# Optimization experiments

Hardware: AMD Instinct MI355X
Metric: run time of the kernel (lower is better)

The kernel has to match this reference:

```python
import jax, jax.numpy as jnp
import numpy as np

TOK, B, DIM, TXT, NT, KS, H = 576, 64, 1024, 512, 1000, 3, 24
SCALE = TXT ** -0.5  # qk_scale = head_dim**-0.5 with head_dim = out_dim = 512


def _layernorm(x, g, b, eps=1e-5):
    m = jnp.mean(x, axis=-1, keepdims=True)
    v = jnp.var(x, axis=-1, keepdims=True)
    return (x - m) * jax.lax.rsqrt(v + eps) * g + b


def _cross_attn(q_in, kv, Wq):
    # q_in: [B,tok,DIM] -> q: [B,tok,TXT]; kv: [B,NT,TXT] serves as both K and V
    q = jnp.einsum('btd,de->bte', q_in, Wq)
    attn = jax.nn.softmax(jnp.einsum('bte,bne->btn', q, kv) * SCALE, axis=-1)
    return jnp.einsum('btn,bne->bte', attn, kv)


def _dwconv(z, w):
    # z: [B,1,H,H], w: [1,1,KS,KS], padding KS//2, stride 1
    return jax.lax.conv_general_dilated(
        z, w, window_strides=(1, 1), padding=((KS // 2, KS // 2), (KS // 2, KS // 2)),
        dimension_numbers=('NCHW', 'OIHW', 'NCHW'))


def setup_inputs() -> dict:
    key = jax.random.key(0)
    ks = jax.random.split(key, 6)
    return {
        'x': jax.random.normal(ks[0], (TOK + 1, B, DIM), jnp.float32),
        'text_fea': jax.random.normal(ks[1], (NT, B, TXT), jnp.float32),
        'ln_q1_g': jnp.ones((DIM,), jnp.float32), 'ln_q1_b': jnp.zeros((DIM,), jnp.float32),
        'ln_q2_g': jnp.ones((DIM,), jnp.float32), 'ln_q2_b': jnp.zeros((DIM,), jnp.float32),
        'ln_kv_g': jnp.ones((TXT,), jnp.float32), 'ln_kv_b': jnp.zeros((TXT,), jnp.float32),
        'Wq1': jax.random.normal(ks[2], (DIM, TXT), jnp.float32) * 0.02,
        'Wq2': jax.random.normal(ks[3], (DIM, TXT), jnp.float32) * 0.02,
        'conv_dw': jax.random.normal(ks[4], (1, 1, KS, KS), jnp.float32) * 0.1,
        'conv_final': jax.random.normal(ks[5], (DIM, TXT), jnp.float32) * 0.02,  # [out,in]
    }


def reference(x, text_fea, ln_q1_g, ln_q1_b, ln_q2_g, ln_q2_b, ln_kv_g, ln_kv_b,
              Wq1, Wq2, conv_dw, conv_final):
    x_cls, xp = x[:1], x[1:]                      # [1,B,DIM], [TOK,B,DIM]
    x_loc = jnp.transpose(xp, (1, 0, 2))          # [B,TOK,DIM]
    kv = _layernorm(jnp.transpose(text_fea, (1, 0, 2)), ln_kv_g, ln_kv_b)  # [B,NT,TXT]

    o1 = _cross_attn(_layernorm(x_loc, ln_q1_g, ln_q1_b), kv, Wq1)  # [B,TOK,TXT]
    o2 = _cross_attn(_layernorm(x_loc, ln_q2_g, ln_q2_b), kv, Wq2)

    x1 = jnp.transpose(o1, (0, 2, 1)).reshape(B, TXT, H, H)
    x2 = jnp.transpose(o2, (0, 2, 1)).reshape(B, TXT, H, H)

    avg_x = jnp.mean(x1, axis=1, keepdims=True)   # [B,1,H,H]
    max_x = jnp.max(x2, axis=1, keepdims=True)
    gate1 = jax.nn.sigmoid(_dwconv(avg_x, conv_dw))
    gate2 = jax.nn.sigmoid(_dwconv(max_x, conv_dw))

    x_se = x1 * gate1 + x2 * gate2                # [B,TXT,H,H]
    y = jnp.einsum('bchw,oc->bohw', x_se, conv_final)  # 1x1 conv, padding 0

    y = jnp.transpose(y.reshape(B, DIM, TOK), (2, 0, 1))  # [TOK,B,DIM]
    return jnp.concatenate([x_cls, y], axis=0)
```

## Files before the change

kernel.cpp:

```cpp
#include <hip/hip_runtime.h>

#define B_    64
#define TOK_  576
#define DIM_  1024
#define TXT_  512
#define NT_   1000
#define NTQ_  1024
#define NTP_  1024
#define H_    24
#define BT_   (B_ * TOK_)
static constexpr float SCALE_ = 0.0441941738241592f;

typedef __bf16 bf16x8 __attribute__((ext_vector_type(8)));
typedef float  f32x4  __attribute__((ext_vector_type(4)));

__device__ __forceinline__ unsigned short f2bf(float f) {
    unsigned u = __float_as_uint(f);
    u += 0x7fffu + ((u >> 16) & 1u);
    return (unsigned short)(u >> 16);
}
__device__ __forceinline__ float bf2f(unsigned short h) {
    return __uint_as_float(((unsigned)h) << 16);
}
__device__ __forceinline__ f32x4 mfma16(bf16x8 a, bf16x8 b, f32x4 c) {
    return __builtin_amdgcn_mfma_f32_16x16x32_bf16(a, b, c, 0, 0, 0);
}
__device__ __forceinline__ void unpack8(uint4 v, float* f) {
    unsigned a0 = v.x, a1 = v.y, a2 = v.z, a3 = v.w;
    f[0] = bf2f((unsigned short)(a0 & 0xffff)); f[1] = bf2f((unsigned short)(a0 >> 16));
    f[2] = bf2f((unsigned short)(a1 & 0xffff)); f[3] = bf2f((unsigned short)(a1 >> 16));
    f[4] = bf2f((unsigned short)(a2 & 0xffff)); f[5] = bf2f((unsigned short)(a2 >> 16));
    f[6] = bf2f((unsigned short)(a3 & 0xffff)); f[7] = bf2f((unsigned short)(a3 >> 16));
}
__device__ __forceinline__ unsigned encmax(float f) {
    unsigned u = __float_as_uint(f);
    return (u & 0x80000000u) ? ~u : (u | 0x80000000u);
}
__device__ __forceinline__ float decmax(unsigned k) {
    unsigned u = (k & 0x80000000u) ? (k ^ 0x80000000u) : ~k;
    return __uint_as_float(u);
}

typedef const __attribute__((address_space(1))) unsigned int* as1_u32p;
typedef __attribute__((address_space(3))) unsigned int* as3_u32p;
__device__ __forceinline__ void gll16(const void* g, void* l) {
    __builtin_amdgcn_global_load_lds((as1_u32p)g, (as3_u32p)l, 16, 0, 0);
}

__global__ void k_prep_wq(const float* __restrict__ wq1, const float* __restrict__ wq2,
                          const float* __restrict__ g1, const float* __restrict__ g2,
                          unsigned short* __restrict__ wqt) {
    __shared__ float tile[64][68];
    int bx = blockIdx.x, t = threadIdx.x;
    int br = bx >> 7, kt = (bx >> 3) & 15, nt = bx & 7;
    const float* wq = br ? wq2 : wq1;
    const float* gg = br ? g2 : g1;
#pragma unroll
    for (int i = 0; i < 4; ++i) {
        int idx4 = t + i * 256;
        int kl = idx4 >> 4, n4 = (idx4 & 15) * 4;
        float gv = gg[kt * 64 + kl];
        float4 v = *reinterpret_cast<const float4*>(wq + (size_t)(kt * 64 + kl) * 512 + nt * 64 + n4);
        tile[kl][n4 + 0] = v.x * gv; tile[kl][n4 + 1] = v.y * gv;
        tile[kl][n4 + 2] = v.z * gv; tile[kl][n4 + 3] = v.w * gv;
    }
    __syncthreads();
#pragma unroll
    for (int i = 0; i < 4; ++i) {
        int idx4 = t + i * 256;
        int nl = idx4 >> 4, k4 = (idx4 & 15) * 4;
        ushort4 o = make_ushort4(f2bf(tile[k4 + 0][nl]), f2bf(tile[k4 + 1][nl]),
                                 f2bf(tile[k4 + 2][nl]), f2bf(tile[k4 + 3][nl]));
        *reinterpret_cast<ushort4*>(wqt + (size_t)br * 512 * 1024 + (size_t)(nt * 64 + nl) * 1024 + kt * 64 + k4) = o;
    }
}

__global__ void k_qbias(const float* __restrict__ wq1, const float* __restrict__ wq2,
                        const float* __restrict__ b1, const float* __restrict__ b2,
                        float* __restrict__ qbias) {
    int br = blockIdx.x >> 3, e0 = (blockIdx.x & 7) * 64;
    int t = threadIdx.x;
    int e = e0 + (t & 63), part = t >> 6;
    const float* wq = br ? wq2 : wq1;
    const float* bb = br ? b2 : b1;
    float s = 0.f;
    for (int d = part * 256; d < part * 256 + 256; ++d) s += bb[d] * wq[(size_t)d * 512 + e];
    __shared__ float red[256];
    red[t] = s;
    __syncthreads();
    if (t < 64) qbias[br * 512 + e0 + t] = red[t] + red[64 + t] + red[128 + t] + red[192 + t];
}

__global__ void k_f2bf(const float* __restrict__ src, unsigned short* __restrict__ dst, int n4) {
    int i = blockIdx.x * blockDim.x + threadIdx.x;
    if (i < n4) {
        float4 v = *reinterpret_cast<const float4*>(src + (size_t)i * 4);
        ushort4 o = make_ushort4(f2bf(v.x), f2bf(v.y), f2bf(v.z), f2bf(v.w));
        *reinterpret_cast<ushort4*>(dst + (size_t)i * 4) = o;
    }
}

__global__ void k_kvln(const float* __restrict__ tf, const float* __restrict__ g,
                       const float* __restrict__ bta, unsigned short* __restrict__ kvn) {
    int row = blockIdx.x;
    int b = row >> 10, n = row & 1023;
    int t = threadIdx.x;
    unsigned short* dst = kvn + ((size_t)b * NTQ_ + n) * TXT_;
    if (n >= NT_) {
        *reinterpret_cast<ushort4*>(dst + t * 4) = make_ushort4(0, 0, 0, 0);
        return;
    }
    const float* src = tf + ((size_t)n * B_ + b) * TXT_;
    float4 v = *reinterpret_cast<const float4*>(src + t * 4);
    float s = v.x + v.y + v.z + v.w;
    float ss = v.x * v.x + v.y * v.y + v.z * v.z + v.w * v.w;
#pragma unroll
    for (int d = 1; d < 64; d <<= 1) { s += __shfl_xor(s, d); ss += __shfl_xor(ss, d); }
    __shared__ float red[4];
    if ((t & 63) == 0) { red[(t >> 6) * 2] = s; red[(t >> 6) * 2 + 1] = ss; }
    __syncthreads();
    s = red[0] + red[2]; ss = red[1] + red[3];
    float m = s * (1.f / TXT_);
    float rs = rsqrtf(ss * (1.f / TXT_) - m * m + 1e-5f);
    int d0 = t * 4;
    ushort4 o = make_ushort4(f2bf((v.x - m) * rs * g[d0 + 0] + bta[d0 + 0]),
                             f2bf((v.y - m) * rs * g[d0 + 1] + bta[d0 + 1]),
                             f2bf((v.z - m) * rs * g[d0 + 2] + bta[d0 + 2]),
                             f2bf((v.w - m) * rs * g[d0 + 3] + bta[d0 + 3]));
    *reinterpret_cast<ushort4*>(dst + d0) = o;
}

__global__ void k_kvt(const unsigned short* __restrict__ kvn, unsigned short* __restrict__ kvt) {
    __shared__ unsigned short tile[64][68];
    int bx = blockIdx.x;
    int b = bx >> 7, rem = bx & 127, et = rem >> 4, nt = rem & 15;
    int t = threadIdx.x;
#pragma unroll
    for (int i = 0; i < 4; ++i) {
        int idx4 = t + i * 256;
        int nl = idx4 >> 4, e4 = (idx4 & 15) * 4;
        int ng = nt * 64 + nl;
        ushort4 v = make_ushort4(0, 0, 0, 0);
        if (ng < NT_) v = *reinterpret_cast<const ushort4*>(kvn + ((size_t)b * NTQ_ + ng) * TXT_ + et * 64 + e4);
        tile[nl][e4 + 0] = v.x; tile[nl][e4 + 1] = v.y; tile[nl][e4 + 2] = v.z; tile[nl][e4 + 3] = v.w;
    }
    __syncthreads();
#pragma unroll
    for (int i = 0; i < 4; ++i) {
        int idx4 = t + i * 256;
        int el = idx4 >> 4, n4 = (idx4 & 15) * 4;
        ushort4 o = make_ushort4(tile[n4 + 0][el], tile[n4 + 1][el], tile[n4 + 2][el], tile[n4 + 3][el]);
        *reinterpret_cast<ushort4*>(kvt + ((size_t)b * TXT_ + et * 64 + el) * NTP_ + nt * 64 + n4) = o;
    }
}

__global__ void k_xln(const float* __restrict__ x, unsigned short* __restrict__ xn) {
    int bt = blockIdx.x;
    int b = bt / TOK_, tk = bt - b * TOK_;
    const float* src = x + ((size_t)(tk + 1) * B_ + b) * DIM_;
    int t = threadIdx.x;
    float4 v = *reinterpret_cast<const float4*>(src + t * 4);
    float s = v.x + v.y + v.z + v.w;
    float ss = v.x * v.x + v.y * v.y + v.z * v.z + v.w * v.w;
#pragma unroll
    for (int d = 1; d < 64; d <<= 1) { s += __shfl_xor(s, d); ss += __shfl_xor(ss, d); }
    __shared__ float red[8];
    if ((t & 63) == 0) { red[t >> 6] = s; red[4 + (t >> 6)] = ss; }
    __syncthreads();
    s = red[0] + red[1] + red[2] + red[3];
    ss = red[4] + red[5] + red[6] + red[7];
    float m = s * (1.f / DIM_);
    float rs = rsqrtf(ss * (1.f / DIM_) - m * m + 1e-5f);
    int d0 = t * 4;
    ushort4 o = make_ushort4(f2bf((v.x - m) * rs), f2bf((v.y - m) * rs),
                             f2bf((v.z - m) * rs), f2bf((v.w - m) * rs));
    *reinterpret_cast<ushort4*>(xn + (size_t)bt * DIM_ + d0) = o;
}

__device__ __forceinline__ void gemm_loop_gll(const unsigned short* __restrict__ A,
                                              const unsigned short* __restrict__ Bp,
                                              int K, unsigned short* a_lds, unsigned short* b_lds,
                                              int tid, f32x4 acc[4][4]) {
    const int l = tid & 63, w = tid >> 6;
    const int l16 = l & 15, lg = l >> 4;
    const int wm = w & 1, wn = w >> 1;
    const f32x4 fz = {0.f, 0.f, 0.f, 0.f};
#pragma unroll
    for (int mt = 0; mt < 4; ++mt)
#pragma unroll
        for (int nt = 0; nt < 4; ++nt) acc[mt][nt] = fz;
    const int lrow = l >> 3;
    const int k8g = (l & 7) ^ lrow;
    const int nk = K >> 6;
    for (int kt = 0; kt < nk; ++kt) {
#pragma unroll
        for (int i = 0; i < 4; ++i) {
            int row = i * 32 + w * 8 + lrow;
            gll16(A + (size_t)row * K + kt * 64 + k8g * 8, &a_lds[(i * 256 + w * 64) * 8]);
        }
#pragma unroll
        for (int i = 0; i < 4; ++i) {
            int row = i * 32 + w * 8 + lrow;
            gll16(Bp + (size_t)row * K + kt * 64 + k8g * 8, &b_lds[(i * 256 + w * 64) * 8]);
        }
        __syncthreads();
#pragma unroll
        for (int kk = 0; kk < 2; ++kk) {
            bf16x8 af[4], bff[4];
#pragma unroll
            for (int mt = 0; mt < 4; ++mt) {
                int row = wm * 64 + mt * 16 + l16;
                int gs = (kk * 4 + lg) ^ (row & 7);
                af[mt] = *reinterpret_cast<const bf16x8*>(a_lds + row * 64 + gs * 8);
            }
#pragma unroll
            for (int nt = 0; nt < 4; ++nt) {
                int row = wn * 64 + nt * 16 + l16;
                int gs = (kk * 4 + lg) ^ (row & 7);
                bff[nt] = *reinterpret_cast<const bf16x8*>(b_lds + row * 64 + gs * 8);
            }
#pragma unroll
            for (int mt = 0; mt < 4; ++mt)
#pragma unroll
                for (int nt = 0; nt < 4; ++nt)
                    acc[mt][nt] = mfma16(af[mt], bff[nt], acc[mt][nt]);
        }
        __syncthreads();
    }
}

__device__ __forceinline__ void gemm_loop96(const unsigned short* __restrict__ A,
                                            const unsigned short* __restrict__ Bp,
                                            int K, unsigned short* a_lds, unsigned short* b_lds,
                                            int tid, f32x4 acc[3][4]) {
    const int l = tid & 63, w = tid >> 6;
    const int l16 = l & 15, lg = l >> 4;
    const int wm = w & 1, wn = w >> 1;
    const f32x4 fz = {0.f, 0.f, 0.f, 0.f};
#pragma unroll
    for (int mt = 0; mt < 3; ++mt)
#pragma unroll
        for (int nt = 0; nt < 4; ++nt) acc[mt][nt] = fz;
    const int lrow = l >> 3;
    const int k8g = (l & 7) ^ lrow;
    const int nk = K >> 6;
    for (int kt = 0; kt < nk; ++kt) {
#pragma unroll
        for (int i = 0; i < 3; ++i) {
            int row = i * 32 + w * 8 + lrow;
            gll16(A + (size_t)row * K + kt * 64 + k8g * 8, &a_lds[(i * 256 + w * 64) * 8]);
        }
#pragma unroll
        for (int i = 0; i < 4; ++i) {
            int row = i * 32 + w * 8 + lrow;
            gll16(Bp + (size_t)row * K + kt * 64 + k8g * 8, &b_lds[(i * 256 + w * 64) * 8]);
        }
        __syncthreads();
#pragma unroll
        for (int kk = 0; kk < 2; ++kk) {
            bf16x8 af[3], bff[4];
#pragma unroll
            for (int mt = 0; mt < 3; ++mt) {
                int row = wm * 48 + mt * 16 + l16;
                int gs = (kk * 4 + lg) ^ (row & 7);
                af[mt] = *reinterpret_cast<const bf16x8*>(a_lds + row * 64 + gs * 8);
            }
#pragma unroll
            for (int nt = 0; nt < 4; ++nt) {
                int row = wn * 64 + nt * 16 + l16;
                int gs = (kk * 4 + lg) ^ (row & 7);
                bff[nt] = *reinterpret_cast<const bf16x8*>(b_lds + row * 64 + gs * 8);
            }
#pragma unroll
            for (int mt = 0; mt < 3; ++mt)
#pragma unroll
                for (int nt = 0; nt < 4; ++nt)
                    acc[mt][nt] = mfma16(af[mt], bff[nt], acc[mt][nt]);
        }
        __syncthreads();
    }
}

__global__ __launch_bounds__(256, 4) void k_qgemm(const unsigned short* __restrict__ xn,
                                                  const unsigned short* __restrict__ wqt,
                                                  const float* __restrict__ qbias,
                                                  unsigned short* __restrict__ qb) {
    int bid = blockIdx.x;
    int vb = (bid & 7) * 288 + (bid >> 3);
    int bn = vb & 3;
    int t = vb >> 2;
    int br = (t >= 288) ? 1 : 0;
    int bm = t - br * 288;
    const unsigned short* A = xn + (size_t)bm * 128 * DIM_;
    const unsigned short* Bp = wqt + (size_t)br * 512 * 1024 + (size_t)bn * 128 * 1024;
    unsigned short* C = qb + (size_t)br * BT_ * TXT_;
    const float* bias = qbias + br * 512;
    __shared__ unsigned short a_lds[128 * 64];
    __shared__ unsigned short b_lds[128 * 64];
    f32x4 acc[4][4];
    gemm_loop_gll(A, Bp, DIM_, a_lds, b_lds, threadIdx.x, acc);
    const int l = threadIdx.x & 63, w = threadIdx.x >> 6;
    const int l16 = l & 15, lg = l >> 4, wm = w & 1, wn = w >> 1;
#pragma unroll
    for (int mt = 0; mt < 4; ++mt)
#pragma unroll
        for (int nt = 0; nt < 4; ++nt) {
            int col = bn * 128 + wn * 64 + nt * 16 + l16;
            float bv = bias[col];
#pragma unroll
            for (int r = 0; r < 4; ++r) {
                int row = bm * 128 + wm * 64 + mt * 16 + lg * 4 + r;
                C[(size_t)row * TXT_ + col] = f2bf((acc[mt][nt][r] + bv) * SCALE_);
            }
        }
}

__global__ __launch_bounds__(256, 4) void k_score(const unsigned short* __restrict__ qbuf,
                                                  const unsigned short* __restrict__ kvn,
                                                  unsigned short* __restrict__ P,
                                                  float* __restrict__ denom, int br) {
    int bid = blockIdx.x;
    int vb = (bid & 7) * 384 + (bid >> 3);
    int tile = vb % 48, b = vb / 48;
    int mt = tile >> 3, nt = tile & 7;
    const unsigned short* A = qbuf + ((size_t)br * BT_ + (size_t)b * TOK_ + mt * 96) * TXT_;
    const unsigned short* Bp = kvn + (size_t)b * NTQ_ * TXT_ + (size_t)nt * 128 * TXT_;
    __shared__ unsigned short a_lds[96 * 64];
    __shared__ unsigned short b_lds[128 * 64];
    f32x4 acc[3][4];
    gemm_loop96(A, Bp, TXT_, a_lds, b_lds, threadIdx.x, acc);
    const int l = threadIdx.x & 63, w = threadIdx.x >> 6;
    const int l16 = l & 15, lg = l >> 4, wm = w & 1, wn = w >> 1;
    float* dn = denom + (size_t)br * BT_;
#pragma unroll
    for (int mt2 = 0; mt2 < 3; ++mt2)
#pragma unroll
        for (int r = 0; r < 4; ++r) {
            int row = b * TOK_ + mt * 96 + wm * 48 + mt2 * 16 + lg * 4 + r;
            float s = 0.f;
#pragma unroll
            for (int nt2 = 0; nt2 < 4; ++nt2) {
                int col = nt * 128 + wn * 64 + nt2 * 16 + l16;
                float p = (col < NT_) ? __expf(acc[mt2][nt2][r]) : 0.f;
                s += p;
                P[(size_t)row * NTP_ + col] = f2bf(p);
            }
#pragma unroll
            for (int d = 1; d < 16; d <<= 1) s += __shfl_xor(s, d);
            if (l16 == 0) atomicAdd(&dn[row], s);
        }
}

__global__ __launch_bounds__(256, 4) void k_pv(const unsigned short* __restrict__ P,
                                               const unsigned short* __restrict__ kvt,
                                               const float* __restrict__ denom,
                                               unsigned short* __restrict__ ob,
                                               float* __restrict__ avgs,
                                               unsigned* __restrict__ maxe, int br) {
    int bid = blockIdx.x;
    int vb = (bid & 7) * 192 + (bid >> 3);
    int tile = vb % 24, b = vb / 24;
    int mt = tile >> 2, nt = tile & 3;
    const unsigned short* A = P + ((size_t)b * TOK_ + mt * 96) * NTP_;
    const unsigned short* Bp = kvt + (size_t)b * TXT_ * NTP_ + (size_t)nt * 128 * NTP_;
    __shared__ unsigned short a_lds[96 * 64];
    __shared__ unsigned short b_lds[128 * 64];
    f32x4 acc[3][4];
    gemm_loop96(A, Bp, NTP_, a_lds, b_lds, threadIdx.x, acc);
    const int l = threadIdx.x & 63, w = threadIdx.x >> 6;
    const int l16 = l & 15, lg = l >> 4, wm = w & 1, wn = w >> 1;
    const float* dn = denom + (size_t)br * BT_;
#pragma unroll
    for (int mt2 = 0; mt2 < 3; ++mt2)
#pragma unroll
        for (int r = 0; r < 4; ++r) {
            int row = b * TOK_ + mt * 96 + wm * 48 + mt2 * 16 + lg * 4 + r;
            float inv = 1.f / dn[row];
            unsigned short* dst = ob + ((size_t)br * BT_ + row) * TXT_;
            float sum = 0.f, mx = -1e30f;
#pragma unroll
            for (int nt2 = 0; nt2 < 4; ++nt2) {
                int col = nt * 128 + wn * 64 + nt2 * 16 + l16;
                float o = acc[mt2][nt2][r] * inv;
                dst[col] = f2bf(o);
                sum += o;
                mx = fmaxf(mx, o);
            }
#pragma unroll
            for (int d = 1; d < 16; d <<= 1) {
                sum += __shfl_xor(sum, d);
                mx = fmaxf(mx, __shfl_xor(mx, d));
            }
            if (l16 == 0) {
                if (br == 0) atomicAdd(&avgs[row], sum);
                else         atomicMax(&maxe[row], encmax(mx));
            }
        }
}

__global__ __launch_bounds__(256, 4) void k_fgemm(const unsigned short* __restrict__ xse,
                                                  const unsigned short* __restrict__ wfb,
                                                  float* __restrict__ out) {
    int bid = blockIdx.x;
    int vb = (bid & 7) * 288 + (bid >> 3);
    int bn = vb & 7, bm = vb >> 3;
    const unsigned short* A = xse + (size_t)bm * 128 * TXT_;
    const unsigned short* Bp = wfb + (size_t)bn * 128 * TXT_;
    __shared__ unsigned short a_lds[128 * 64];
    __shared__ unsigned short b_lds[128 * 64];
    f32x4 acc[4][4];
    gemm_loop_gll(A, Bp, TXT_, a_lds, b_lds, threadIdx.x, acc);
    const int l = threadIdx.x & 63, w = threadIdx.x >> 6;
    const int l16 = l & 15, lg = l >> 4, wm = w & 1, wn = w >> 1;
#pragma unroll
    for (int mt = 0; mt < 4; ++mt)
#pragma unroll
        for (int r = 0; r < 4; ++r) {
            int rowg = bm * 128 + wm * 64 + mt * 16 + lg * 4 + r;
            int b = rowg / TOK_, tk = rowg - b * TOK_;
            float* dst = out + ((size_t)(tk + 1) * B_ + b) * DIM_;
#pragma unroll
            for (int nt = 0; nt < 4; ++nt) {
                int col = bn * 128 + wn * 64 + nt * 16 + l16;
                dst[col] = acc[mt][nt][r];
            }
        }
}

__global__ void k_xse(const unsigned short* __restrict__ o1, const unsigned short* __restrict__ o2,
                      const float* __restrict__ avgs, const unsigned* __restrict__ maxe,
                      const float* __restrict__ cdw, unsigned short* __restrict__ xse) {
    int idx8 = blockIdx.x * 256 + threadIdx.x;
    int bt = idx8 >> 6, e8 = threadIdx.x & 63;
    float gg1 = 0.f, gg2 = 0.f;
    if (e8 == 0) {
        int b = bt / TOK_, hw = bt - b * TOK_, h = hw / H_, ww = hw - h * H_;
        float a1 = 0.f, a2 = 0.f;
#pragma unroll
        for (int ky = 0; ky < 3; ++ky)
#pragma unroll
            for (int kx = 0; kx < 3; ++kx) {
                int hh = h + ky - 1, wx = ww + kx - 1;
                if (hh >= 0 && hh < H_ && wx >= 0 && wx < H_) {
                    float wv = cdw[ky * 3 + kx];
                    int s = b * TOK_ + hh * H_ + wx;
                    a1 += wv * avgs[s] * (1.f / TXT_);
                    a2 += wv * decmax(maxe[s]);
                }
            }
        gg1 = 1.f / (1.f + __expf(-a1));
        gg2 = 1.f / (1.f + __expf(-a2));
    }
    gg1 = __shfl(gg1, 0);
    gg2 = __shfl(gg2, 0);
    float f1[8], f2[8];
    unpack8(*reinterpret_cast<const uint4*>(o1 + (size_t)bt * TXT_ + e8 * 8), f1);
    unpack8(*reinterpret_cast<const uint4*>(o2 + (size_t)bt * TXT_ + e8 * 8), f2);
    unsigned r[4];
#pragma unroll
    for (int j = 0; j < 4; ++j) {
        unsigned lo = f2bf(f1[2 * j] * gg1 + f2[2 * j] * gg2);
        unsigned hi = f2bf(f1[2 * j + 1] * gg1 + f2[2 * j + 1] * gg2);
        r[j] = lo | (hi << 16);
    }
    uint4 o = make_uint4(r[0], r[1], r[2], r[3]);
    *reinterpret_cast<uint4*>(xse + (size_t)bt * TXT_ + e8 * 8) = o;
}

extern "C" void kernel_launch(void* const* d_in, const int* in_sizes, int n_in,
                              void* d_out, int out_size, void* d_ws, size_t ws_size,
                              hipStream_t stream) {
    (void)in_sizes; (void)n_in; (void)out_size; (void)ws_size;
    const float* x    = (const float*)d_in[0];
    const float* tf   = (const float*)d_in[1];
    const float* lq1g = (const float*)d_in[2];
    const float* lq1b = (const float*)d_in[3];
    const float* lq2g = (const float*)d_in[4];
    const float* lq2b = (const float*)d_in[5];
    const float* lkvg = (const float*)d_in[6];
    const float* lkvb = (const float*)d_in[7];
    const float* wq1  = (const float*)d_in[8];
    const float* wq2  = (const float*)d_in[9];
    const float* cdw  = (const float*)d_in[10];
    const float* wf   = (const float*)d_in[11];
    float* out = (float*)d_out;

    char* ws = (char*)d_ws;
    size_t off = 0;
    auto carve = [&](size_t bytes) { char* p = ws + off; off += (bytes + 255) & ~(size_t)255; return p; };
    unsigned short* kvn  = (unsigned short*)carve((size_t)B_ * NTQ_ * TXT_ * 2);
    unsigned short* kvt  = (unsigned short*)carve((size_t)B_ * TXT_ * NTP_ * 2);
    unsigned short* wqt  = (unsigned short*)carve((size_t)2 * 512 * 1024 * 2);
    unsigned short* wfb  = (unsigned short*)carve((size_t)1024 * 512 * 2);
    float* qbias = (float*)carve((size_t)2 * 512 * 4);
    float* denom = (float*)carve((size_t)2 * BT_ * 4);
    float* avgs  = (float*)carve((size_t)BT_ * 4);
    unsigned* maxe = (unsigned*)carve((size_t)BT_ * 4);
    unsigned short* xn   = (unsigned short*)carve((size_t)BT_ * DIM_ * 2);
    unsigned short* qbuf = (unsigned short*)carve((size_t)2 * BT_ * TXT_ * 2);
    unsigned short* ob   = (unsigned short*)carve((size_t)2 * BT_ * TXT_ * 2);
    unsigned short* Pm   = xn;
    unsigned short* xse  = qbuf;

    hipMemcpyAsync(out, x, (size_t)B_ * DIM_ * sizeof(float), hipMemcpyDeviceToDevice, stream);

    k_prep_wq<<<256, 256, 0, stream>>>(wq1, wq2, lq1g, lq2g, wqt);
    k_qbias<<<16, 256, 0, stream>>>(wq1, wq2, lq1b, lq2b, qbias);
    k_f2bf<<<512, 256, 0, stream>>>(wf, wfb, 131072);
    k_kvln<<<B_ * NTQ_, 128, 0, stream>>>(tf, lkvg, lkvb, kvn);
    k_kvt<<<8192, 256, 0, stream>>>(kvn, kvt);
    k_xln<<<BT_, 256, 0, stream>>>(x, xn);
    k_qgemm<<<2304, 256, 0, stream>>>(xn, wqt, qbias, qbuf);
    hipMemsetAsync(denom, 0, (size_t)2 * BT_ * 4, stream);
    hipMemsetAsync(avgs, 0, (size_t)BT_ * 4, stream);
    hipMemsetAsync(maxe, 0, (size_t)BT_ * 4, stream);
    k_score<<<3072, 256, 0, stream>>>(qbuf, kvn, Pm, denom, 0);
    k_pv<<<1536, 256, 0, stream>>>(Pm, kvt, denom, ob, avgs, maxe, 0);
    k_score<<<3072, 256, 0, stream>>>(qbuf, kvn, Pm, denom, 1);
    k_pv<<<1536, 256, 0, stream>>>(Pm, kvt, denom, ob, avgs, maxe, 1);
    k_xse<<<9216, 256, 0, stream>>>(ob, ob + (size_t)BT_ * TXT_, avgs, maxe, cdw, xse);
    k_fgemm<<<2304, 256, 0, stream>>>(xse, wfb, out);
}
```

Before: 636.9 us.

## Fuse gating into final GEMM A-load and use wave-per-row layernorms

Removes the separate xse kernel. The final 1x1-conv GEMM now computes the sigmoid gates per row, loads o1/o2 directly, blends them and writes the bf16 result into LDS as its A tile. This avoids writing and re-reading the xse intermediate. The two layernorm kernels now process one row per wavefront, with 8 rows per block and no LDS reduction or barrier. The three memsets are merged into one. The cost is that A loads become synchronous register loads instead of direct global-to-LDS loads, and the gates are recomputed once per column block (8 times per row).

Result: no change. 635.3 us (-0.3%).

```diff
diff --git a/kernel.cpp b/kernel.cpp
--- a/kernel.cpp
+++ b/kernel.cpp
@@ -100,34 +100,35 @@
     }
 }
 
-__global__ void k_kvln(const float* __restrict__ tf, const float* __restrict__ g,
-                       const float* __restrict__ bta, unsigned short* __restrict__ kvn) {
-    int row = blockIdx.x;
+__global__ __launch_bounds__(512, 2) void k_kvln(const float* __restrict__ tf, const float* __restrict__ g,
+                                                 const float* __restrict__ bta, unsigned short* __restrict__ kvn) {
+    int row = blockIdx.x * 8 + (threadIdx.x >> 6);
     int b = row >> 10, n = row & 1023;
-    int t = threadIdx.x;
-    unsigned short* dst = kvn + ((size_t)b * NTQ_ + n) * TXT_;
+    int l = threadIdx.x & 63;
+    unsigned short* dst = kvn + ((size_t)b * NTQ_ + n) * TXT_ + l * 8;
     if (n >= NT_) {
-        *reinterpret_cast<ushort4*>(dst + t * 4) = make_ushort4(0, 0, 0, 0);
+        *reinterpret_cast<uint4*>(dst) = make_uint4(0, 0, 0, 0);
         return;
     }
-    const float* src = tf + ((size_t)n * B_ + b) * TXT_;
-    float4 v = *reinterpret_cast<const float4*>(src + t * 4);
-    float s = v.x + v.y + v.z + v.w;
-    float ss = v.x * v.x + v.y * v.y + v.z * v.z + v.w * v.w;
+    const float* src = tf + ((size_t)n * B_ + b) * TXT_ + l * 8;
+    float4 v0 = *reinterpret_cast<const float4*>(src);
+    float4 v1 = *reinterpret_cast<const float4*>(src + 4);
+    float s  = v0.x + v0.y + v0.z + v0.w + v1.x + v1.y + v1.z + v1.w;
+    float ss = v0.x * v0.x + v0.y * v0.y + v0.z * v0.z + v0.w * v0.w
+             + v1.x * v1.x + v1.y * v1.y + v1.z * v1.z + v1.w * v1.w;
 #pragma unroll
     for (int d = 1; d < 64; d <<= 1) { s += __shfl_xor(s, d); ss += __shfl_xor(ss, d); }
-    __shared__ float red[4];
-    if ((t & 63) == 0) { red[(t >> 6) * 2] = s; red[(t >> 6) * 2 + 1] = ss; }
-    __syncthreads();
-    s = red[0] + red[2]; ss = red[1] + red[3];
     float m = s * (1.f / TXT_);
     float rs = rsqrtf(ss * (1.f / TXT_) - m * m + 1e-5f);
-    int d0 = t * 4;
-    ushort4 o = make_ushort4(f2bf((v.x - m) * rs * g[d0 + 0] + bta[d0 + 0]),
-                             f2bf((v.y - m) * rs * g[d0 + 1] + bta[d0 + 1]),
-                             f2bf((v.z - m) * rs * g[d0 + 2] + bta[d0 + 2]),
-                             f2bf((v.w - m) * rs * g[d0 + 3] + bta[d0 + 3]));
-    *reinterpret_cast<ushort4*>(dst + d0) = o;
+    float4 g0 = *reinterpret_cast<const float4*>(g + l * 8);
+    float4 g1 = *reinterpret_cast<const float4*>(g + l * 8 + 4);
+    float4 b0 = *reinterpret_cast<const float4*>(bta + l * 8);
+    float4 b1 = *reinterpret_cast<const float4*>(bta + l * 8 + 4);
+    unsigned r0 = (unsigned)f2bf((v0.x - m) * rs * g0.x + b0.x) | ((unsigned)f2bf((v0.y - m) * rs * g0.y + b0.y) << 16);
+    unsigned r1 = (unsigned)f2bf((v0.z - m) * rs * g0.z + b0.z) | ((unsigned)f2bf((v0.w - m) * rs * g0.w + b0.w) << 16);
+    unsigned r2 = (unsigned)f2bf((v1.x - m) * rs * g1.x + b1.x) | ((unsigned)f2bf((v1.y - m) * rs * g1.y + b1.y) << 16);
+    unsigned r3 = (unsigned)f2bf((v1.z - m) * rs * g1.z + b1.z) | ((unsigned)f2bf((v1.w - m) * rs * g1.w + b1.w) << 16);
+    *reinterpret_cast<uint4*>(dst) = make_uint4(r0, r1, r2, r3);
 }
 
 __global__ void k_kvt(const unsigned short* __restrict__ kvn, unsigned short* __restrict__ kvt) {
@@ -154,27 +155,33 @@
     }
 }
 
-__global__ void k_xln(const float* __restrict__ x, unsigned short* __restrict__ xn) {
-    int bt = blockIdx.x;
+__global__ __launch_bounds__(512, 2) void k_xln(const float* __restrict__ x, unsigned short* __restrict__ xn) {
+    int bt = blockIdx.x * 8 + (threadIdx.x >> 6);
     int b = bt / TOK_, tk = bt - b * TOK_;
-    const float* src = x + ((size_t)(tk + 1) * B_ + b) * DIM_;
-    int t = threadIdx.x;
-    float4 v = *reinterpret_cast<const float4*>(src + t * 4);
-    float s = v.x + v.y + v.z + v.w;
-    float ss = v.x * v.x + v.y * v.y + v.z * v.z + v.w * v.w;
+    int l = threadIdx.x & 63;
+    const float* src = x + ((size_t)(tk + 1) * B_ + b) * DIM_ + l * 16;
+    float4 v[4];
+#pragma unroll
+    for (int j = 0; j < 4; ++j) v[j] = *reinterpret_cast<const float4*>(src + j * 4);
+    float s = 0.f, ss = 0.f;
+#pragma unroll
+    for (int j = 0; j < 4; ++j) {
+        s += v[j].x + v[j].y + v[j].z + v[j].w;
+        ss += v[j].x * v[j].x + v[j].y * v[j].y + v[j].z * v[j].z + v[j].w * v[j].w;
+    }
 #pragma unroll
     for (int d = 1; d < 64; d <<= 1) { s += __shfl_xor(s, d); ss += __shfl_xor(ss, d); }
-    __shared__ float red[8];
-    if ((t & 63) == 0) { red[t >> 6] = s; red[4 + (t >> 6)] = ss; }
-    __syncthreads();
-    s = red[0] + red[1] + red[2] + red[3];
-    ss = red[4] + red[5] + red[6] + red[7];
     float m = s * (1.f / DIM_);
     float rs = rsqrtf(ss * (1.f / DIM_) - m * m + 1e-5f);
-    int d0 = t * 4;
-    ushort4 o = make_ushort4(f2bf((v.x - m) * rs), f2bf((v.y - m) * rs),
-                             f2bf((v.z - m) * rs), f2bf((v.w - m) * rs));
-    *reinterpret_cast<ushort4*>(xn + (size_t)bt * DIM_ + d0) = o;
+    unsigned short* dst = xn + (size_t)bt * DIM_ + l * 16;
+#pragma unroll
+    for (int h = 0; h < 2; ++h) {
+        unsigned r0 = (unsigned)f2bf((v[2*h].x - m) * rs) | ((unsigned)f2bf((v[2*h].y - m) * rs) << 16);
+        unsigned r1 = (unsigned)f2bf((v[2*h].z - m) * rs) | ((unsigned)f2bf((v[2*h].w - m) * rs) << 16);
+        unsigned r2 = (unsigned)f2bf((v[2*h+1].x - m) * rs) | ((unsigned)f2bf((v[2*h+1].y - m) * rs) << 16);
+        unsigned r3 = (unsigned)f2bf((v[2*h+1].z - m) * rs) | ((unsigned)f2bf((v[2*h+1].w - m) * rs) << 16);
+        *reinterpret_cast<uint4*>(dst + h * 8) = make_uint4(r0, r1, r2, r3);
+    }
 }
 
 __device__ __forceinline__ void gemm_loop_gll(const unsigned short* __restrict__ A,
@@ -398,43 +405,24 @@
         }
 }
 
-__global__ __launch_bounds__(256, 4) void k_fgemm(const unsigned short* __restrict__ xse,
-                                                  const unsigned short* __restrict__ wfb,
-                                                  float* __restrict__ out) {
+__global__ __launch_bounds__(256, 4) void k_fgemm2(const unsigned short* __restrict__ o1,
+                                                   const unsigned short* __restrict__ o2,
+                                                   const float* __restrict__ avgs,
+                                                   const unsigned* __restrict__ maxe,
+                                                   const float* __restrict__ cdw,
+                                                   const unsigned short* __restrict__ wfb,
+                                                   float* __restrict__ out) {
     int bid = blockIdx.x;
     int vb = (bid & 7) * 288 + (bid >> 3);
     int bn = vb & 7, bm = vb >> 3;
-    const unsigned short* A = xse + (size_t)bm * 128 * TXT_;
     const unsigned short* Bp = wfb + (size_t)bn * 128 * TXT_;
     __shared__ unsigned short a_lds[128 * 64];
     __shared__ unsigned short b_lds[128 * 64];
-    f32x4 acc[4][4];
-    gemm_loop_gll(A, Bp, TXT_, a_lds, b_lds, threadIdx.x, acc);
-    const int l = threadIdx.x & 63, w = threadIdx.x >> 6;
-    const int l16 = l & 15, lg = l >> 4, wm = w & 1, wn = w >> 1;
-#pragma unroll
-    for (int mt = 0; mt < 4; ++mt)
-#pragma unroll
-        for (int r = 0; r < 4; ++r) {
-            int rowg = bm * 128 + wm * 64 + mt * 16 + lg * 4 + r;
-            int b = rowg / TOK_, tk = rowg - b * TOK_;
-            float* dst = out + ((size_t)(tk + 1) * B_ + b) * DIM_;
-#pragma unroll
-            for (int nt = 0; nt < 4; ++nt) {
-                int col = bn * 128 + wn * 64 + nt * 16 + l16;
-                dst[col] = acc[mt][nt][r];
-            }
-        }
-}
-
-__global__ void k_xse(const unsigned short* __restrict__ o1, const unsigned short* __restrict__ o2,
-                      const float* __restrict__ avgs, const unsigned* __restrict__ maxe,
-                      const float* __restrict__ cdw, unsigned short* __restrict__ xse) {
-    int idx8 = blockIdx.x * 256 + threadIdx.x;
-    int bt = idx8 >> 6, e8 = threadIdx.x & 63;
-    float gg1 = 0.f, gg2 = 0.f;
-    if (e8 == 0) {
-        int b = bt / TOK_, hw = bt - b * TOK_, h = hw / H_, ww = hw - h * H_;
+    __shared__ float glds[128][2];
+    const int tid = threadIdx.x;
+    if (tid < 128) {
+        int rowg = bm * 128 + tid;
+        int b = rowg / TOK_, hw = rowg - b * TOK_, h = hw / H_, ww = hw - h * H_;
         float a1 = 0.f, a2 = 0.f;
 #pragma unroll
         for (int ky = 0; ky < 3; ++ky)
@@ -448,23 +436,83 @@
                     a2 += wv * decmax(maxe[s]);
                 }
             }
-        gg1 = 1.f / (1.f + __expf(-a1));
-        gg2 = 1.f / (1.f + __expf(-a2));
-    }
-    gg1 = __shfl(gg1, 0);
-    gg2 = __shfl(gg2, 0);
-    float f1[8], f2[8];
-    unpack8(*reinterpret_cast<const uint4*>(o1 + (size_t)bt * TXT_ + e8 * 8), f1);
-    unpack8(*reinterpret_cast<const uint4*>(o2 + (size_t)bt * TXT_ + e8 * 8), f2);
-    unsigned r[4];
-#pragma unroll
-    for (int j = 0; j < 4; ++j) {
-        unsigned lo = f2bf(f1[2 * j] * gg1 + f2[2 * j] * gg2);
-        unsigned hi = f2bf(f1[2 * j + 1] * gg1 + f2[2 * j + 1] * gg2);
-        r[j] = lo | (hi << 16);
-    }
-    uint4 o = make_uint4(r[0], r[1], r[2], r[3]);
-    *reinterpret_cast<uint4*>(xse + (size_t)bt * TXT_ + e8 * 8) = o;
+        glds[tid][0] = 1.f / (1.f + __expf(-a1));
+        glds[tid][1] = 1.f / (1.f + __expf(-a2));
+    }
+    __syncthreads();
+    const int l = tid & 63, w = tid >> 6;
+    const int l16 = l & 15, lg = l >> 4;
+    const int wm = w & 1, wn = w >> 1;
+    const f32x4 fz = {0.f, 0.f, 0.f, 0.f};
+    f32x4 acc[4][4];
+#pragma unroll
+    for (int mt = 0; mt < 4; ++mt)
+#pragma unroll
+        for (int nt = 0; nt < 4; ++nt) acc[mt][nt] = fz;
+    const int lrow = l >> 3;
+    const int k8g = (l & 7) ^ lrow;
+    const int gA = l & 7;
+    for (int kt = 0; kt < 8; ++kt) {
+#pragma unroll
+        for (int i = 0; i < 4; ++i) {
+            int row = i * 32 + w * 8 + lrow;
+            size_t goff = (size_t)(bm * 128 + row) * TXT_ + kt * 64 + gA * 8;
+            uint4 va = *reinterpret_cast<const uint4*>(o1 + goff);
+            uint4 vb2 = *reinterpret_cast<const uint4*>(o2 + goff);
+            float f1[8], f2[8];
+            unpack8(va, f1); unpack8(vb2, f2);
+            float gg1 = glds[row][0], gg2 = glds[row][1];
+            unsigned rr[4];
+#pragma unroll
+            for (int j = 0; j < 4; ++j) {
+                unsigned lo = f2bf(f1[2 * j] * gg1 + f2[2 * j] * gg2);
+                unsigned hi = f2bf(f1[2 * j + 1] * gg1 + f2[2 * j + 1] * gg2);
+                rr[j] = lo | (hi << 16);
+            }
+            *reinterpret_cast<uint4*>(a_lds + row * 64 + (gA ^ (row & 7)) * 8) = make_uint4(rr[0], rr[1], rr[2], rr[3]);
+        }
+#pragma unroll
+        for (int i = 0; i < 4; ++i) {
+            int row = i * 32 + w * 8 + lrow;
+            gll16(Bp + (size_t)row * TXT_ + kt * 64 + k8g * 8, &b_lds[(i * 256 + w * 64) * 8]);
+        }
+        __syncthreads();
+#pragma unroll
+        for (int kk = 0; kk < 2; ++kk) {
+            bf16x8 af[4], bff[4];
+#pragma unroll
+            for (int mt = 0; mt < 4; ++mt) {
+                int row = wm * 64 + mt * 16 + l16;
+                int gs = (kk * 4 + lg) ^ (row & 7);
+                af[mt] = *reinterpret_cast<const bf16x8*>(a_lds + row * 64 + gs * 8);
+            }
+#pragma unroll
+            for (int nt = 0; nt < 4; ++nt) {
+                int row = wn * 64 + nt * 16 + l16;
+                int gs = (kk * 4 + lg) ^ (row & 7);
+                bff[nt] = *reinterpret_cast<const bf16x8*>(b_lds + row * 64 + gs * 8);
+            }
+#pragma unroll
+            for (int mt = 0; mt < 4; ++mt)
+#pragma unroll
+                for (int nt = 0; nt < 4; ++nt)
+                    acc[mt][nt] = mfma16(af[mt], bff[nt], acc[mt][nt]);
+        }
+        __syncthreads();
+    }
+#pragma unroll
+    for (int mt = 0; mt < 4; ++mt)
+#pragma unroll
+        for (int r = 0; r < 4; ++r) {
+            int rowg = bm * 128 + wm * 64 + mt * 16 + lg * 4 + r;
+            int b = rowg / TOK_, tk = rowg - b * TOK_;
+            float* dst = out + ((size_t)(tk + 1) * B_ + b) * DIM_;
+#pragma unroll
+            for (int nt = 0; nt < 4; ++nt) {
+                int col = bn * 128 + wn * 64 + nt * 16 + l16;
+                dst[col] = acc[mt][nt][r];
+            }
+        }
 }
 
 extern "C" void kernel_launch(void* const* d_in, const int* in_sizes, int n_in,
@@ -493,31 +541,28 @@
     unsigned short* wqt  = (unsigned short*)carve((size_t)2 * 512 * 1024 * 2);
     unsigned short* wfb  = (unsigned short*)carve((size_t)1024 * 512 * 2);
     float* qbias = (float*)carve((size_t)2 * 512 * 4);
-    float* denom = (float*)carve((size_t)2 * BT_ * 4);
-    float* avgs  = (float*)carve((size_t)BT_ * 4);
-    unsigned* maxe = (unsigned*)carve((size_t)BT_ * 4);
+    float* stats = (float*)carve((size_t)4 * BT_ * 4);
+    float* denom = stats;
+    float* avgs  = stats + 2 * BT_;
+    unsigned* maxe = (unsigned*)(stats + 3 * BT_);
     unsigned short* xn   = (unsigned short*)carve((size_t)BT_ * DIM_ * 2);
     unsigned short* qbuf = (unsigned short*)carve((size_t)2 * BT_ * TXT_ * 2);
     unsigned short* ob   = (unsigned short*)carve((size_t)2 * BT_ * TXT_ * 2);
     unsigned short* Pm   = xn;
-    unsigned short* xse  = qbuf;
 
     hipMemcpyAsync(out, x, (size_t)B_ * DIM_ * sizeof(float), hipMemcpyDeviceToDevice, stream);
 
     k_prep_wq<<<256, 256, 0, stream>>>(wq1, wq2, lq1g, lq2g, wqt);
     k_qbias<<<16, 256, 0, stream>>>(wq1, wq2, lq1b, lq2b, qbias);
     k_f2bf<<<512, 256, 0, stream>>>(wf, wfb, 131072);
-    k_kvln<<<B_ * NTQ_, 128, 0, stream>>>(tf, lkvg, lkvb, kvn);
+    k_kvln<<<8192, 512, 0, stream>>>(tf, lkvg, lkvb, kvn);
     k_kvt<<<8192, 256, 0, stream>>>(kvn, kvt);
-    k_xln<<<BT_, 256, 0, stream>>>(x, xn);
+    k_xln<<<4608, 512, 0, stream>>>(x, xn);
     k_qgemm<<<2304, 256, 0, stream>>>(xn, wqt, qbias, qbuf);
-    hipMemsetAsync(denom, 0, (size_t)2 * BT_ * 4, stream);
-    hipMemsetAsync(avgs, 0, (size_t)BT_ * 4, stream);
-    hipMemsetAsync(maxe, 0, (size_t)BT_ * 4, stream);
+    hipMemsetAsync(stats, 0, (size_t)4 * BT_ * 4, stream);
     k_score<<<3072, 256, 0, stream>>>(qbuf, kvn, Pm, denom, 0);
     k_pv<<<1536, 256, 0, stream>>>(Pm, kvt, denom, ob, avgs, maxe, 0);
     k_score<<<3072, 256, 0, stream>>>(qbuf, kvn, Pm, denom, 1);
     k_pv<<<1536, 256, 0, stream>>>(Pm, kvt, denom, ob, avgs, maxe, 1);
-    k_xse<<<9216, 256, 0, stream>>>(ob, ob + (size_t)BT_ * TXT_, avgs, maxe, cdw, xse);
-    k_fgemm<<<2304, 256, 0, stream>>>(xse, wfb, out);
-}
+    k_fgemm2<<<2304, 256, 0, stream>>>(ob, ob + (size_t)BT_ * TXT_, avgs, maxe, cdw, wfb, out);
+}
```
